# Kernel optimization log

Measured on AMD Instinct MI355X. Metric: run time of the kernel, lower is better.

Reference implementation:

```python
import jax, jax.numpy as jnp
import numpy as np

B, T_ENC, T_DEC = 8, 256, 256
ENC_DIM, DEC_UNITS = 512, 256


def setup_inputs() -> dict:
    key = jax.random.key(0)
    ks = jax.random.split(key, 6)
    s1 = 1.0 / np.sqrt(ENC_DIM)
    s2 = 1.0 / np.sqrt(DEC_UNITS)
    return {
        "enc_outputs": jax.random.normal(ks[0], (B, T_ENC, ENC_DIM), jnp.float32),
        "dec_outputs": jax.random.normal(ks[1], (B, T_DEC, DEC_UNITS), jnp.float32),
        "W1": jax.random.normal(ks[2], (ENC_DIM, DEC_UNITS), jnp.float32) * s1,
        "b1": jnp.zeros((DEC_UNITS,), jnp.float32),
        "W2": jax.random.normal(ks[3], (DEC_UNITS, DEC_UNITS), jnp.float32) * s2,
        "b2": jnp.zeros((DEC_UNITS,), jnp.float32),
        "Vw": jax.random.normal(ks[4], (DEC_UNITS,), jnp.float32) * s2,
        "Vb": jnp.zeros((1,), jnp.float32),
    }


def reference(enc_outputs, dec_outputs, W1, b1, W2, b2, Vw, Vb):
    # proj_enc: (B, T_enc, U); proj_dec: (B, T_dec, U)
    proj_enc = jnp.einsum("bte,eu->btu", enc_outputs, W1) + b1
    proj_dec = jnp.einsum("bsd,du->bsu", dec_outputs, W2) + b2
    # broadcast add -> (B, T_dec, T_enc, U), tanh, then contract with Vw -> score (B, T_dec, T_enc)
    hidden = jnp.tanh(proj_dec[:, :, None, :] + proj_enc[:, None, :, :])
    score = jnp.einsum("bstu,u->bst", hidden, Vw) + Vb[0]
    attention_weights = jax.nn.softmax(score, axis=-1)
    # context: (B, T_dec, enc_dim)
    context = jnp.einsum("bst,bte->bse", attention_weights, enc_outputs)
    return (context, attention_weights)
```

## Files before the change

kernel.cpp:

```cpp
#include <hip/hip_runtime.h>

#define NB 8
#define TE 256
#define TD 256
#define ED 512
#define DU 256


__global__ __launch_bounds__(256) void proj_exp_kernel(
    const float* __restrict__ enc, const float* __restrict__ dec,
    const float* __restrict__ W1, const float* __restrict__ b1,
    const float* __restrict__ W2, const float* __restrict__ b2,
    float* __restrict__ Epd, float* __restrict__ EpeT2)
{
  __shared__ __align__(16) float As[32][34];
  __shared__ __align__(16) float Bs[32][64];
  const int blk = blockIdx.x;
  const bool is_pe = blk < 256;
  const int sub = blk & 255;
  const int K = is_pe ? ED : DU;
  const int NT = K >> 5;
  const float* __restrict__ A = is_pe ? enc : dec;
  const float* __restrict__ W = is_pe ? W1 : W2;
  const float* __restrict__ bias = is_pe ? b1 : b2;
  const int mt = sub >> 2, nt = sub & 3;
  const int m0 = mt * 32, n0 = nt * 64;
  const int tid = threadIdx.x;
  const int tx = tid & 15, ty = tid >> 4;
  const int at = tid >> 3, ka = (tid & 7) << 2;
  const int kb = tid >> 4, jb = (tid & 15) << 2;

  const float* __restrict__ Ap = A + (size_t)(m0 + at) * K + ka;
  const float* __restrict__ Wp = W + (size_t)kb * DU + n0 + jb;

  float acc[2][4] = {};
  float4 aV, wV0, wV1;

  auto loadr = [&](int k0) {
    aV = *(const float4*)(Ap + k0);
    wV0 = *(const float4*)(Wp + (size_t)k0 * DU);
    wV1 = *(const float4*)(Wp + (size_t)(k0 + 16) * DU);
  };

  loadr(0);
  for (int kt = 0; kt < NT; ++kt) {
    As[ka + 0][at] = aV.x;
    As[ka + 1][at] = aV.y;
    As[ka + 2][at] = aV.z;
    As[ka + 3][at] = aV.w;
    *(float4*)&Bs[kb][jb] = wV0;
    *(float4*)&Bs[kb + 16][jb] = wV1;
    __syncthreads();
    if (kt + 1 < NT) loadr((kt + 1) << 5);
#pragma unroll
    for (int kk = 0; kk < 32; ++kk) {
      const float2 a2 = *(const float2*)&As[kk][ty * 2];
      const float4 w4 = *(const float4*)&Bs[kk][tx * 4];
      acc[0][0] = fmaf(a2.x, w4.x, acc[0][0]);
      acc[0][1] = fmaf(a2.x, w4.y, acc[0][1]);
      acc[0][2] = fmaf(a2.x, w4.z, acc[0][2]);
      acc[0][3] = fmaf(a2.x, w4.w, acc[0][3]);
      acc[1][0] = fmaf(a2.y, w4.x, acc[1][0]);
      acc[1][1] = fmaf(a2.y, w4.y, acc[1][1]);
      acc[1][2] = fmaf(a2.y, w4.z, acc[1][2]);
      acc[1][3] = fmaf(a2.y, w4.w, acc[1][3]);
    }
    __syncthreads();
  }

  const float4 bv4 = *(const float4*)(bias + n0 + tx * 4);
  const float bvv[4] = {bv4.x, bv4.y, bv4.z, bv4.w};
  if (is_pe) {
    const int b = m0 >> 8, t0 = m0 & 255;
    const int uqg = (b << 6) + (n0 >> 2) + tx;
    const int tg = t0 + ty * 2;
    float* dst = EpeT2 + ((size_t)uqg << 10) + (tg << 2);
    float4 o0, o1;
    o0.x = __expf(2.0f * (acc[0][0] + bvv[0]));
    o0.y = __expf(2.0f * (acc[0][1] + bvv[1]));
    o0.z = __expf(2.0f * (acc[0][2] + bvv[2]));
    o0.w = __expf(2.0f * (acc[0][3] + bvv[3]));
    o1.x = __expf(2.0f * (acc[1][0] + bvv[0]));
    o1.y = __expf(2.0f * (acc[1][1] + bvv[1]));
    o1.z = __expf(2.0f * (acc[1][2] + bvv[2]));
    o1.w = __expf(2.0f * (acc[1][3] + bvv[3]));
    *(float4*)dst = o0;
    *(float4*)(dst + 4) = o1;
  } else {
#pragma unroll
    for (int r = 0; r < 2; ++r) {
      const int m = m0 + ty * 2 + r;
      float4 o;
      o.x = __expf(2.0f * (acc[r][0] + bvv[0]));
      o.y = __expf(2.0f * (acc[r][1] + bvv[1]));
      o.z = __expf(2.0f * (acc[r][2] + bvv[2]));
      o.w = __expf(2.0f * (acc[r][3] + bvv[3]));
      *(float4*)(Epd + ((size_t)m << 8) + n0 + tx * 4) = o;
    }
  }
}

__global__ __launch_bounds__(512) void score_ctx_kernel(
    const float* __restrict__ Epd, const float* __restrict__ EpeT2,
    const float* __restrict__ Vw, const float* __restrict__ enc,
    float* __restrict__ attn, float* __restrict__ ctx)
{
  __shared__ __align__(16) float eps[4 * 256];
  __shared__ __align__(16) float vws[256];
  __shared__ __align__(16) float comb[4][256];
  __shared__ __align__(16) float att[4][256];
  __shared__ float redm[4][4];
  __shared__ float reds[4][4];

  const int blk0 = blockIdx.x;
  const int blk = ((blk0 & 7) << 6) | (blk0 >> 3);
  const int b = blk >> 6;
  const int s0 = (blk & 63) << 2;
  const int tid = threadIdx.x;
  const int t = tid & 255;
  const int h = tid >> 8;

  if (h == 0) {
    ((float4*)eps)[t] =
        ((const float4*)(Epd + (((size_t)((b << 8) + s0)) << 8)))[t];
  } else if (t < 64) {
    ((float4*)vws)[t] = ((const float4*)Vw)[t];
  }
  __syncthreads();

  const float* __restrict__ ep =
      EpeT2 + ((size_t)b << 16) + ((size_t)h << 15) + (t << 2);
  const int qb = h << 5;

  float a0 = 0.f, a1 = 0.f, a2 = 0.f, a3 = 0.f;
#pragma unroll 4
  for (int q = 0; q < 32; ++q) {
    const int u4 = (qb + q) << 2;
    const float4 vw = *(const float4*)&vws[u4];
    const float4 e0 = *(const float4*)&eps[u4];
    const float4 e1 = *(const float4*)&eps[256 + u4];
    const float4 e2 = *(const float4*)&eps[512 + u4];
    const float4 e3 = *(const float4*)&eps[768 + u4];
    const float4 g = *(const float4*)(ep + ((size_t)q << 10));
    a0 = fmaf(vw.x, __builtin_amdgcn_rcpf(fmaf(e0.x, g.x, 1.0f)), a0);
    a1 = fmaf(vw.x, __builtin_amdgcn_rcpf(fmaf(e1.x, g.x, 1.0f)), a1);
    a2 = fmaf(vw.x, __builtin_amdgcn_rcpf(fmaf(e2.x, g.x, 1.0f)), a2);
    a3 = fmaf(vw.x, __builtin_amdgcn_rcpf(fmaf(e3.x, g.x, 1.0f)), a3);
    a0 = fmaf(vw.y, __builtin_amdgcn_rcpf(fmaf(e0.y, g.y, 1.0f)), a0);
    a1 = fmaf(vw.y, __builtin_amdgcn_rcpf(fmaf(e1.y, g.y, 1.0f)), a1);
    a2 = fmaf(vw.y, __builtin_amdgcn_rcpf(fmaf(e2.y, g.y, 1.0f)), a2);
    a3 = fmaf(vw.y, __builtin_amdgcn_rcpf(fmaf(e3.y, g.y, 1.0f)), a3);
    a0 = fmaf(vw.z, __builtin_amdgcn_rcpf(fmaf(e0.z, g.z, 1.0f)), a0);
    a1 = fmaf(vw.z, __builtin_amdgcn_rcpf(fmaf(e1.z, g.z, 1.0f)), a1);
    a2 = fmaf(vw.z, __builtin_amdgcn_rcpf(fmaf(e2.z, g.z, 1.0f)), a2);
    a3 = fmaf(vw.z, __builtin_amdgcn_rcpf(fmaf(e3.z, g.z, 1.0f)), a3);
    a0 = fmaf(vw.w, __builtin_amdgcn_rcpf(fmaf(e0.w, g.w, 1.0f)), a0);
    a1 = fmaf(vw.w, __builtin_amdgcn_rcpf(fmaf(e1.w, g.w, 1.0f)), a1);
    a2 = fmaf(vw.w, __builtin_amdgcn_rcpf(fmaf(e2.w, g.w, 1.0f)), a2);
    a3 = fmaf(vw.w, __builtin_amdgcn_rcpf(fmaf(e3.w, g.w, 1.0f)), a3);
  }

  if (h == 1) {
    comb[0][t] = a0;
    comb[1][t] = a1;
    comb[2][t] = a2;
    comb[3][t] = a3;
  }
  __syncthreads();

  const int wid = tid >> 6, lane = tid & 63;
  float v[4], e[4];
  if (h == 0) {
    v[0] = -2.f * (a0 + comb[0][t]);
    v[1] = -2.f * (a1 + comb[1][t]);
    v[2] = -2.f * (a2 + comb[2][t]);
    v[3] = -2.f * (a3 + comb[3][t]);
#pragma unroll
    for (int r = 0; r < 4; ++r) {
      float m = v[r];
#pragma unroll
      for (int off = 32; off; off >>= 1) m = fmaxf(m, __shfl_xor(m, off));
      if (lane == 0) redm[r][wid] = m;
    }
  }
  __syncthreads();
  if (h == 0) {
#pragma unroll
    for (int r = 0; r < 4; ++r) {
      const float m = fmaxf(fmaxf(redm[r][0], redm[r][1]),
                            fmaxf(redm[r][2], redm[r][3]));
      e[r] = __expf(v[r] - m);
      float s = e[r];
#pragma unroll
      for (int off = 32; off; off >>= 1) s += __shfl_xor(s, off);
      if (lane == 0) reds[r][wid] = s;
    }
  }
  __syncthreads();
  if (h == 0) {
#pragma unroll
    for (int r = 0; r < 4; ++r) {
      const float s = (reds[r][0] + reds[r][1]) + (reds[r][2] + reds[r][3]);
      const float p = e[r] * __builtin_amdgcn_rcpf(s);
      attn[(((size_t)((b << 8) + s0 + r)) << 8) + t] = p;
      att[r][t] = p;
    }
  }
  __syncthreads();

  const int c = tid;
  const float* __restrict__ encb = enc + ((size_t)b << 17) + c;
  float acc0 = 0.f, acc1 = 0.f, acc2 = 0.f, acc3 = 0.f;
#pragma unroll 2
  for (int t0 = 0; t0 < 256; t0 += 4) {
    const float4 p0 = *(const float4*)&att[0][t0];
    const float4 p1 = *(const float4*)&att[1][t0];
    const float4 p2 = *(const float4*)&att[2][t0];
    const float4 p3 = *(const float4*)&att[3][t0];
    const float pv0[4] = {p0.x, p0.y, p0.z, p0.w};
    const float pv1[4] = {p1.x, p1.y, p1.z, p1.w};
    const float pv2[4] = {p2.x, p2.y, p2.z, p2.w};
    const float pv3[4] = {p3.x, p3.y, p3.z, p3.w};
#pragma unroll
    for (int i = 0; i < 4; ++i) {
      const float ev = encb[(size_t)(t0 + i) << 9];
      acc0 = fmaf(pv0[i], ev, acc0);
      acc1 = fmaf(pv1[i], ev, acc1);
      acc2 = fmaf(pv2[i], ev, acc2);
      acc3 = fmaf(pv3[i], ev, acc3);
    }
  }
  float* __restrict__ cb = ctx + (((size_t)((b << 8) + s0)) << 9) + c;
  cb[0 * ED] = acc0;
  cb[1 * ED] = acc1;
  cb[2 * ED] = acc2;
  cb[3 * ED] = acc3;
}

extern "C" void kernel_launch(void* const* d_in, const int* in_sizes, int n_in,
                              void* d_out, int out_size, void* d_ws, size_t ws_size,
                              hipStream_t stream) {
  const float* enc = (const float*)d_in[0];
  const float* dec = (const float*)d_in[1];
  const float* W1 = (const float*)d_in[2];
  const float* b1 = (const float*)d_in[3];
  const float* W2 = (const float*)d_in[4];
  const float* b2 = (const float*)d_in[5];
  const float* Vw = (const float*)d_in[6];

  float* ctx = (float*)d_out;
  float* attn = (float*)d_out + (size_t)NB * TD * ED;
  float* Epd = (float*)d_ws;
  float* EpeT2 = Epd + (size_t)NB * TD * DU;

  proj_exp_kernel<<<dim3(512), dim3(256), 0, stream>>>(enc, dec, W1, b1, W2,
                                                       b2, Epd, EpeT2);
  score_ctx_kernel<<<dim3(512), dim3(512), 0, stream>>>(Epd, EpeT2, Vw, enc,
                                                        attn, ctx);
}
```

Before: 54.82 us.

## Split-K the projection GEMM across two thread halves and prefetch score loads

The projection kernel now runs 512 threads per block. Each half accumulates half of the K dimension in its own shared tiles, and the partial sums are combined through shared memory before the exp epilogue. The goal is more parallelism and latency hiding in a GEMM with only 512 small blocks. In the score kernel, the next EpeT2 float4 is loaded one iteration ahead to hide global-load latency. The cost is extra shared memory and a reduction barrier, which may lower occupancy.

```diff
diff --git a/kernel.cpp b/kernel.cpp
--- a/kernel.cpp
+++ b/kernel.cpp
@@ -7,31 +7,35 @@
 #define DU 256
 
 
-__global__ __launch_bounds__(256) void proj_exp_kernel(
+__global__ __launch_bounds__(512) void proj_exp_kernel(
     const float* __restrict__ enc, const float* __restrict__ dec,
     const float* __restrict__ W1, const float* __restrict__ b1,
     const float* __restrict__ W2, const float* __restrict__ b2,
     float* __restrict__ Epd, float* __restrict__ EpeT2)
 {
-  __shared__ __align__(16) float As[32][34];
-  __shared__ __align__(16) float Bs[32][64];
+  __shared__ __align__(16) float As[2][32][34];
+  __shared__ __align__(16) float Bs[2][32][64];
+  __shared__ __align__(16) float comb[8][256];
   const int blk = blockIdx.x;
   const bool is_pe = blk < 256;
   const int sub = blk & 255;
   const int K = is_pe ? ED : DU;
-  const int NT = K >> 5;
+  const int NTh = K >> 6;
   const float* __restrict__ A = is_pe ? enc : dec;
   const float* __restrict__ W = is_pe ? W1 : W2;
   const float* __restrict__ bias = is_pe ? b1 : b2;
   const int mt = sub >> 2, nt = sub & 3;
   const int m0 = mt * 32, n0 = nt * 64;
   const int tid = threadIdx.x;
-  const int tx = tid & 15, ty = tid >> 4;
-  const int at = tid >> 3, ka = (tid & 7) << 2;
-  const int kb = tid >> 4, jb = (tid & 15) << 2;
-
-  const float* __restrict__ Ap = A + (size_t)(m0 + at) * K + ka;
-  const float* __restrict__ Wp = W + (size_t)kb * DU + n0 + jb;
+  const int t = tid & 255;
+  const int h = tid >> 8;
+  const int k0base = h * (K >> 1);
+  const int tx = t & 15, ty = t >> 4;
+  const int at = t >> 3, ka = (t & 7) << 2;
+  const int kb = t >> 4, jb = (t & 15) << 2;
+
+  const float* __restrict__ Ap = A + (size_t)(m0 + at) * K + k0base + ka;
+  const float* __restrict__ Wp = W + (size_t)(k0base + kb) * DU + n0 + jb;
 
   float acc[2][4] = {};
   float4 aV, wV0, wV1;
@@ -43,19 +47,19 @@
   };
 
   loadr(0);
-  for (int kt = 0; kt < NT; ++kt) {
-    As[ka + 0][at] = aV.x;
-    As[ka + 1][at] = aV.y;
-    As[ka + 2][at] = aV.z;
-    As[ka + 3][at] = aV.w;
-    *(float4*)&Bs[kb][jb] = wV0;
-    *(float4*)&Bs[kb + 16][jb] = wV1;
+  for (int kt = 0; kt < NTh; ++kt) {
+    As[h][ka + 0][at] = aV.x;
+    As[h][ka + 1][at] = aV.y;
+    As[h][ka + 2][at] = aV.z;
+    As[h][ka + 3][at] = aV.w;
+    *(float4*)&Bs[h][kb][jb] = wV0;
+    *(float4*)&Bs[h][kb + 16][jb] = wV1;
     __syncthreads();
-    if (kt + 1 < NT) loadr((kt + 1) << 5);
+    if (kt + 1 < NTh) loadr((kt + 1) << 5);
 #pragma unroll
     for (int kk = 0; kk < 32; ++kk) {
-      const float2 a2 = *(const float2*)&As[kk][ty * 2];
-      const float4 w4 = *(const float4*)&Bs[kk][tx * 4];
+      const float2 a2 = *(const float2*)&As[h][kk][ty * 2];
+      const float4 w4 = *(const float4*)&Bs[h][kk][tx * 4];
       acc[0][0] = fmaf(a2.x, w4.x, acc[0][0]);
       acc[0][1] = fmaf(a2.x, w4.y, acc[0][1]);
       acc[0][2] = fmaf(a2.x, w4.z, acc[0][2]);
@@ -68,34 +72,48 @@
     __syncthreads();
   }
 
-  const float4 bv4 = *(const float4*)(bias + n0 + tx * 4);
-  const float bvv[4] = {bv4.x, bv4.y, bv4.z, bv4.w};
-  if (is_pe) {
-    const int b = m0 >> 8, t0 = m0 & 255;
-    const int uqg = (b << 6) + (n0 >> 2) + tx;
-    const int tg = t0 + ty * 2;
-    float* dst = EpeT2 + ((size_t)uqg << 10) + (tg << 2);
-    float4 o0, o1;
-    o0.x = __expf(2.0f * (acc[0][0] + bvv[0]));
-    o0.y = __expf(2.0f * (acc[0][1] + bvv[1]));
-    o0.z = __expf(2.0f * (acc[0][2] + bvv[2]));
-    o0.w = __expf(2.0f * (acc[0][3] + bvv[3]));
-    o1.x = __expf(2.0f * (acc[1][0] + bvv[0]));
-    o1.y = __expf(2.0f * (acc[1][1] + bvv[1]));
-    o1.z = __expf(2.0f * (acc[1][2] + bvv[2]));
-    o1.w = __expf(2.0f * (acc[1][3] + bvv[3]));
-    *(float4*)dst = o0;
-    *(float4*)(dst + 4) = o1;
-  } else {
-#pragma unroll
-    for (int r = 0; r < 2; ++r) {
-      const int m = m0 + ty * 2 + r;
-      float4 o;
-      o.x = __expf(2.0f * (acc[r][0] + bvv[0]));
-      o.y = __expf(2.0f * (acc[r][1] + bvv[1]));
-      o.z = __expf(2.0f * (acc[r][2] + bvv[2]));
-      o.w = __expf(2.0f * (acc[r][3] + bvv[3]));
-      *(float4*)(Epd + ((size_t)m << 8) + n0 + tx * 4) = o;
+  if (h == 1) {
+#pragma unroll
+    for (int r = 0; r < 2; ++r)
+#pragma unroll
+      for (int j = 0; j < 4; ++j) comb[r * 4 + j][t] = acc[r][j];
+  }
+  __syncthreads();
+  if (h == 0) {
+#pragma unroll
+    for (int r = 0; r < 2; ++r)
+#pragma unroll
+      for (int j = 0; j < 4; ++j) acc[r][j] += comb[r * 4 + j][t];
+
+    const float4 bv4 = *(const float4*)(bias + n0 + tx * 4);
+    const float bvv[4] = {bv4.x, bv4.y, bv4.z, bv4.w};
+    if (is_pe) {
+      const int b = m0 >> 8, t0 = m0 & 255;
+      const int uqg = (b << 6) + (n0 >> 2) + tx;
+      const int tg = t0 + ty * 2;
+      float* dst = EpeT2 + ((size_t)uqg << 10) + (tg << 2);
+      float4 o0, o1;
+      o0.x = __expf(2.0f * (acc[0][0] + bvv[0]));
+      o0.y = __expf(2.0f * (acc[0][1] + bvv[1]));
+      o0.z = __expf(2.0f * (acc[0][2] + bvv[2]));
+      o0.w = __expf(2.0f * (acc[0][3] + bvv[3]));
+      o1.x = __expf(2.0f * (acc[1][0] + bvv[0]));
+      o1.y = __expf(2.0f * (acc[1][1] + bvv[1]));
+      o1.z = __expf(2.0f * (acc[1][2] + bvv[2]));
+      o1.w = __expf(2.0f * (acc[1][3] + bvv[3]));
+      *(float4*)dst = o0;
+      *(float4*)(dst + 4) = o1;
+    } else {
+#pragma unroll
+      for (int r = 0; r < 2; ++r) {
+        const int m = m0 + ty * 2 + r;
+        float4 o;
+        o.x = __expf(2.0f * (acc[r][0] + bvv[0]));
+        o.y = __expf(2.0f * (acc[r][1] + bvv[1]));
+        o.z = __expf(2.0f * (acc[r][2] + bvv[2]));
+        o.w = __expf(2.0f * (acc[r][3] + bvv[3]));
+        *(float4*)(Epd + ((size_t)m << 8) + n0 + tx * 4) = o;
+      }
     }
   }
 }
@@ -133,15 +151,17 @@
   const int qb = h << 5;
 
   float a0 = 0.f, a1 = 0.f, a2 = 0.f, a3 = 0.f;
+  float4 g = *(const float4*)ep;
 #pragma unroll 4
   for (int q = 0; q < 32; ++q) {
+    float4 gn;
+    if (q + 1 < 32) gn = *(const float4*)(ep + ((size_t)(q + 1) << 10));
     const int u4 = (qb + q) << 2;
     const float4 vw = *(const float4*)&vws[u4];
     const float4 e0 = *(const float4*)&eps[u4];
     const float4 e1 = *(const float4*)&eps[256 + u4];
     const float4 e2 = *(const float4*)&eps[512 + u4];
     const float4 e3 = *(const float4*)&eps[768 + u4];
-    const float4 g = *(const float4*)(ep + ((size_t)q << 10));
     a0 = fmaf(vw.x, __builtin_amdgcn_rcpf(fmaf(e0.x, g.x, 1.0f)), a0);
     a1 = fmaf(vw.x, __builtin_amdgcn_rcpf(fmaf(e1.x, g.x, 1.0f)), a1);
     a2 = fmaf(vw.x, __builtin_amdgcn_rcpf(fmaf(e2.x, g.x, 1.0f)), a2);
@@ -158,6 +178,7 @@
     a1 = fmaf(vw.w, __builtin_amdgcn_rcpf(fmaf(e1.w, g.w, 1.0f)), a1);
     a2 = fmaf(vw.w, __builtin_amdgcn_rcpf(fmaf(e2.w, g.w, 1.0f)), a2);
     a3 = fmaf(vw.w, __builtin_amdgcn_rcpf(fmaf(e3.w, g.w, 1.0f)), a3);
+    g = gn;
   }
 
   if (h == 1) {
@@ -253,7 +274,7 @@
   float* Epd = (float*)d_ws;
   float* EpeT2 = Epd + (size_t)NB * TD * DU;
 
-  proj_exp_kernel<<<dim3(512), dim3(256), 0, stream>>>(enc, dec, W1, b1, W2,
+  proj_exp_kernel<<<dim3(512), dim3(512), 0, stream>>>(enc, dec, W1, b1, W2,
                                                        b2, Epd, EpeT2);
   score_ctx_kernel<<<dim3(512), dim3(512), 0, stream>>>(Epd, EpeT2, Vw, enc,
                                                         attn, ctx);
```

Result: no change. 53.91 us (-1.7%).
